# Kernel tuning notes

Measured on AMD Instinct MI355X. Metric: run time of the kernel, lower is better.

## Reference

```python
import jax, jax.numpy as jnp
import numpy as np

HEADS = 12
WH = WW = 7
N = WH * WW  # 49 tokens per window
NW = 64      # windows per image (mask groups)


def _relative_position_index():
    ch, cw = np.meshgrid(np.arange(WH), np.arange(WW), indexing='ij')
    coords = np.stack([ch, cw]).reshape(2, -1)  # [2, N]
    rel = coords[:, :, None] - coords[:, None, :]  # [2, N, N]
    rel = rel.transpose(1, 2, 0)
    rel[:, :, 0] += WH - 1
    rel[:, :, 1] += WW - 1
    rel[:, :, 0] *= 2 * WW - 1
    return rel.sum(-1).astype(np.int32)  # [N, N]


def setup_inputs() -> dict:
    key = jax.random.key(0)
    ks = jax.random.split(key, 6)
    B, C = 4096, 384
    x = jax.random.normal(ks[0], (B, N, C), dtype=jnp.float32)
    mask = jnp.where(jax.random.uniform(ks[1], (NW, N, N)) > 0.5, 0.0, -100.0).astype(jnp.float32)
    W_qkv = jax.random.normal(ks[2], (C, 3 * C), dtype=jnp.float32) * 0.02
    b_qkv = jnp.zeros((3 * C,), dtype=jnp.float32)
    W_out = jax.random.normal(ks[3], (C, C), dtype=jnp.float32) * 0.02
    b_out = jnp.zeros((C,), dtype=jnp.float32)
    rpb_table = jax.random.normal(ks[4], ((2 * WH - 1) * (2 * WW - 1), HEADS), dtype=jnp.float32) * 0.01
    rel_index = jnp.asarray(_relative_position_index())
    return {"x": x, "mask": mask, "W_qkv": W_qkv, "b_qkv": b_qkv,
            "W_out": W_out, "b_out": b_out, "rpb_table": rpb_table,
            "rel_index": rel_index}


def reference(x, mask, W_qkv, b_qkv, W_out, b_out, rpb_table, rel_index):
    B, n, C = x.shape
    hd = C // HEADS
    scale = hd ** (-0.5)
    qkv = x @ W_qkv + b_qkv                      # [B, n, 3C]
    q, k, v = jnp.split(qkv, 3, axis=2)
    def heads(t):
        return t.reshape(B, n, HEADS, hd).transpose(0, 2, 1, 3)  # b h n d
    q = heads(q) * scale
    k = heads(k)
    v = heads(v)
    attn = jnp.einsum('bhmc,bhnc->bhmn', q, k)   # [B, h, n, n]
    bias = rpb_table[rel_index.reshape(-1)].reshape(n, n, HEADS).transpose(2, 0, 1)
    attn = attn + bias[None]
    nw = mask.shape[0]
    attn = attn.reshape(B // nw, nw, HEADS, n, n) + mask[None, :, None]
    attn = attn.reshape(B, HEADS, n, n)
    attn = jax.nn.softmax(attn, axis=3)
    out = jnp.einsum('bhmn,bhnc->bhmc', attn, v)  # [B, h, n, d]
    out = out.transpose(0, 2, 1, 3).reshape(B, n, C)
    return out @ W_out + b_out
```

## Files before the change

kernel.cpp:

```cpp
#include <hip/hip_runtime.h>

#define NTOK 49
#define CDIM 384
#define HEADS 12
#define HD 32
#define NWIN 64
#define NQKV 1152
#define SCALE 0.17677669529663687f

typedef __attribute__((ext_vector_type(8))) __bf16 bf16x8;
typedef __attribute__((ext_vector_type(4))) float f32x4;

#define OFF_WQKVT   0ull
#define OFF_WOUTT   884736ull
#define OFF_ADDEND  1179648ull
#define OFF_QKVB    8555520ull
#define OFF_ATTNOUT 470977536ull
#define OFF_XB      OFF_ATTNOUT

__device__ __forceinline__ void async_copy16(__bf16* lds_dst, const __bf16* g_src) {
    __builtin_amdgcn_global_load_lds(
        (const __attribute__((address_space(1))) void*)g_src,
        (__attribute__((address_space(3))) void*)lds_dst,
        16, 0, 0);
}


__global__ void prep_weights(const float* __restrict__ Wqkv, const float* __restrict__ Wout,
                             __bf16* __restrict__ WqkvT, __bf16* __restrict__ WoutT) {
    int idx = blockIdx.x * 256 + threadIdx.x;
    if (idx < NQKV * CDIM) {
        int n = idx / CDIM, k = idx % CDIM;
        WqkvT[idx] = (__bf16)Wqkv[(size_t)k * NQKV + n];
    }
    if (idx < CDIM * CDIM) {
        int n = idx / CDIM, k = idx % CDIM;
        WoutT[idx] = (__bf16)Wout[(size_t)k * CDIM + n];
    }
}

__global__ void prep_addend(const float* __restrict__ rpb, const int* __restrict__ rel,
                            const float* __restrict__ mask, float* __restrict__ addend) {
    int idx = blockIdx.x * 256 + threadIdx.x;
    if (idx >= NWIN * HEADS * NTOK * NTOK) return;
    int mn = idx % (NTOK * NTOK);
    int h  = (idx / (NTOK * NTOK)) % HEADS;
    int w  = idx / (NTOK * NTOK * HEADS);
    addend[idx] = rpb[rel[mn] * HEADS + h] + mask[(size_t)w * NTOK * NTOK + mn];
}

__global__ __launch_bounds__(256) void prep_xb(const float* __restrict__ x,
                                               __bf16* __restrict__ xb, int total8) {
    int stride = gridDim.x * 256;
    for (int i = blockIdx.x * 256 + threadIdx.x; i < total8; i += stride) {
        float4 a = reinterpret_cast<const float4*>(x)[i * 2];
        float4 b = reinterpret_cast<const float4*>(x)[i * 2 + 1];
        union { __bf16 h[8]; uint4 u; } t;
        t.h[0] = (__bf16)a.x; t.h[1] = (__bf16)a.y; t.h[2] = (__bf16)a.z; t.h[3] = (__bf16)a.w;
        t.h[4] = (__bf16)b.x; t.h[5] = (__bf16)b.y; t.h[6] = (__bf16)b.z; t.h[7] = (__bf16)b.w;
        reinterpret_cast<uint4*>(xb)[i] = t.u;
    }
}


__global__ __launch_bounds__(256, 3) void gemm_qkv(
    const __bf16* __restrict__ xb, const __bf16* __restrict__ WqkvT,
    const float* __restrict__ bqkv, __bf16* __restrict__ qkvb)
{
    __shared__ __attribute__((aligned(16))) __bf16 smem[16384];
    __bf16* As = smem;
    __bf16* Bs = smem + 8192;

    const int cpx  = 14112 >> 3;
    const int lid  = (blockIdx.x & 7) * cpx + (blockIdx.x >> 3);
    const int mblk = lid / 9, nblk = lid % 9;
    const int n0  = nblk * 128;
    const int bm0 = mblk * 128;

    const int tid = threadIdx.x;
    const int wave = tid >> 6, lane = tid & 63;
    const int l15 = lane & 15, l4 = lane >> 4;
    const int wr = wave >> 1, wc = wave & 1;

    f32x4 acc[4][4] = {};

    for (int k0 = 0; k0 < CDIM; k0 += 64) {
#pragma unroll
        for (int j = 0; j < 4; ++j) {
            int c = wave * 4 + j;
            int mt = c >> 1, kk = c & 1;
            const __bf16* sa = xb + (size_t)(bm0 + mt * 16 + l15) * CDIM + k0 + kk * 32 + l4 * 8;
            async_copy16(&As[c * 512], sa);
            const __bf16* sb = WqkvT + (size_t)(n0 + mt * 16 + l15) * CDIM + k0 + kk * 32 + l4 * 8;
            async_copy16(&Bs[c * 512], sb);
        }
        __syncthreads();

#pragma unroll
        for (int kk = 0; kk < 2; ++kk) {
            bf16x8 af[4], bf[4];
#pragma unroll
            for (int mi = 0; mi < 4; ++mi)
                af[mi] = *reinterpret_cast<const bf16x8*>(&As[((wr * 4 + mi) * 2 + kk) * 512 + lane * 8]);
#pragma unroll
            for (int ni = 0; ni < 4; ++ni)
                bf[ni] = *reinterpret_cast<const bf16x8*>(&Bs[((wc * 4 + ni) * 2 + kk) * 512 + lane * 8]);
#pragma unroll
            for (int mi = 0; mi < 4; ++mi)
#pragma unroll
                for (int ni = 0; ni < 4; ++ni)
                    acc[mi][ni] = __builtin_amdgcn_mfma_f32_16x16x32_bf16(af[mi], bf[ni], acc[mi][ni], 0, 0, 0);
        }
        __syncthreads();
    }

    const float scl = (n0 < CDIM) ? SCALE : 1.0f;
    float bias[4];
#pragma unroll
    for (int ni = 0; ni < 4; ++ni)
        bias[ni] = bqkv[n0 + wc * 64 + ni * 16 + l15];

    __bf16* Cs = smem;
#pragma unroll
    for (int mi = 0; mi < 4; ++mi)
#pragma unroll
        for (int ni = 0; ni < 4; ++ni)
#pragma unroll
            for (int r = 0; r < 4; ++r) {
                int row = wr * 64 + mi * 16 + l4 * 4 + r;
                int col = wc * 64 + ni * 16 + l15;
                int byte = (row * 256 + col * 2) ^ (((row >> 2) & 3) << 5);
                *reinterpret_cast<__bf16*>(reinterpret_cast<char*>(Cs) + byte) =
                    (__bf16)((acc[mi][ni][r] + bias[ni]) * scl);
            }
    __syncthreads();

#pragma unroll
    for (int it = 0; it < 8; ++it) {
        int idx = it * 4096 + tid * 16;
        int row = idx >> 8, bcol = idx & 255;
        int sb = (row * 256 + bcol) ^ (((row >> 2) & 3) << 5);
        uint4 v = *reinterpret_cast<const uint4*>(reinterpret_cast<const char*>(Cs) + sb);
        *reinterpret_cast<uint4*>(reinterpret_cast<char*>(&qkvb[(size_t)(bm0 + row) * NQKV + n0]) + bcol) = v;
    }
}


__global__ __launch_bounds__(256) void attn(
    const __bf16* __restrict__ qkvb, const float* __restrict__ addend,
    __bf16* __restrict__ attnout)
{
    __shared__ __attribute__((aligned(16))) __bf16 ps[4][2][64][8];
    const int b = blockIdx.x;
    const int tid = threadIdx.x;
    const int wave = tid >> 6, lane = tid & 63;
    const int l15 = lane & 15, l4 = lane >> 4;
    const int h = blockIdx.y * 4 + wave;
    const int w = b & (NWIN - 1);

    const __bf16* base = qkvb + (size_t)b * NTOK * NQKV;

    bf16x8 kf[4];
#pragma unroll
    for (int nt = 0; nt < 4; ++nt)
        kf[nt] = *reinterpret_cast<const bf16x8*>(base + (size_t)(nt * 16 + l15) * NQKV + CDIM + h * HD + l4 * 8);

    bf16x8 vf[2][2];
#pragma unroll
    for (int dt = 0; dt < 2; ++dt)
#pragma unroll
        for (int kb = 0; kb < 2; ++kb)
#pragma unroll
            for (int j = 0; j < 8; ++j) {
                int tok = kb * 32 + l4 * 8 + j;
                vf[dt][kb][j] = base[(size_t)tok * NQKV + 2 * CDIM + h * HD + dt * 16 + l15];
            }

    const float* add_h = addend + (size_t)(w * HEADS + h) * (NTOK * NTOK);

    for (int mt = 0; mt < 4; ++mt) {
        bf16x8 qf = *reinterpret_cast<const bf16x8*>(base + (size_t)(mt * 16 + l15) * NQKV + h * HD + l4 * 8);
        f32x4 s[4];
#pragma unroll
        for (int nt = 0; nt < 4; ++nt) {
            f32x4 z = {};
            s[nt] = __builtin_amdgcn_mfma_f32_16x16x32_bf16(qf, kf[nt], z, 0, 0, 0);
        }

#pragma unroll
        for (int r = 0; r < 4; ++r) {
            int m = mt * 16 + l4 * 4 + r;
            float vals[4];
#pragma unroll
            for (int nt = 0; nt < 4; ++nt) {
                int n = nt * 16 + l15;
                float sv = s[nt][r];
                if (n < NTOK) {
                    if (m < NTOK) sv += add_h[m * NTOK + n];
                } else {
                    sv = -1e30f;
                }
                vals[nt] = sv;
            }
            float mx = fmaxf(fmaxf(vals[0], vals[1]), fmaxf(vals[2], vals[3]));
            mx = fmaxf(mx, __shfl_xor(mx, 1));
            mx = fmaxf(mx, __shfl_xor(mx, 2));
            mx = fmaxf(mx, __shfl_xor(mx, 4));
            mx = fmaxf(mx, __shfl_xor(mx, 8));
            float e0 = __expf(vals[0] - mx);
            float e1 = __expf(vals[1] - mx);
            float e2 = __expf(vals[2] - mx);
            float e3 = __expf(vals[3] - mx);
            float sum = (e0 + e1) + (e2 + e3);
            sum += __shfl_xor(sum, 1);
            sum += __shfl_xor(sum, 2);
            sum += __shfl_xor(sum, 4);
            sum += __shfl_xor(sum, 8);
            float inv = 1.0f / sum;
            float ev[4] = {e0, e1, e2, e3};
#pragma unroll
            for (int nt = 0; nt < 4; ++nt) {
                int lp = (l4 * 4 + r) + 16 * ((nt & 1) * 2 + (l15 >> 3));
                ps[wave][nt >> 1][lp][l15 & 7] = (__bf16)(ev[nt] * inv);
            }
        }

        f32x4 o[2] = {};
#pragma unroll
        for (int kb = 0; kb < 2; ++kb) {
            bf16x8 ap = *reinterpret_cast<const bf16x8*>(&ps[wave][kb][lane][0]);
#pragma unroll
            for (int dt = 0; dt < 2; ++dt)
                o[dt] = __builtin_amdgcn_mfma_f32_16x16x32_bf16(ap, vf[dt][kb], o[dt], 0, 0, 0);
        }
#pragma unroll
        for (int dt = 0; dt < 2; ++dt) {
            int col = h * HD + dt * 16 + l15;
#pragma unroll
            for (int r = 0; r < 4; ++r) {
                int tok = mt * 16 + l4 * 4 + r;
                if (tok < NTOK)
                    attnout[((size_t)b * NTOK + tok) * CDIM + col] = (__bf16)o[dt][r];
            }
        }
    }
}


__global__ __launch_bounds__(256, 3) void out_proj(
    const __bf16* __restrict__ A, const __bf16* __restrict__ WoutT,
    const float* __restrict__ bout, float* __restrict__ out)
{
    __shared__ __attribute__((aligned(16))) __bf16 as[4 * 12 * 512];
    const int blk = blockIdx.x, tid = threadIdx.x;
    const int wave = tid >> 6, lane = tid & 63;
    const int l15 = lane & 15, l4 = lane >> 4;

    const __bf16* Ab = A + (size_t)blk * 64 * CDIM;
    for (int i = tid; i < 64 * CDIM / 8; i += 256) {
        int4 ld = reinterpret_cast<const int4*>(Ab)[i];
        int e = i * 8;
        int row = e / CDIM, c = e % CDIM;
        int mt = row >> 4, kb = c >> 5;
        int lp = (row & 15) + 16 * ((c & 31) >> 3);
        int slot = lp ^ (kb & 7);
        *reinterpret_cast<int4*>(&as[((mt * 12 + kb) * 64 + slot) * 8]) = ld;
    }
    __syncthreads();

    f32x4 acc[6][4] = {};
    for (int kb = 0; kb < 12; ++kb) {
        int slot = lane ^ (kb & 7);
        bf16x8 af[4];
#pragma unroll
        for (int mt = 0; mt < 4; ++mt)
            af[mt] = *reinterpret_cast<const bf16x8*>(&as[((mt * 12 + kb) * 64 + slot) * 8]);
#pragma unroll
        for (int j = 0; j < 6; ++j) {
            int col = (wave * 6 + j) * 16 + l15;
            bf16x8 bf = *reinterpret_cast<const bf16x8*>(WoutT + (size_t)col * CDIM + kb * 32 + l4 * 8);
#pragma unroll
            for (int mt = 0; mt < 4; ++mt)
                acc[j][mt] = __builtin_amdgcn_mfma_f32_16x16x32_bf16(af[mt], bf, acc[j][mt], 0, 0, 0);
        }
    }
#pragma unroll
    for (int j = 0; j < 6; ++j) {
        int col = (wave * 6 + j) * 16 + l15;
        float bias = bout[col];
#pragma unroll
        for (int mt = 0; mt < 4; ++mt) {
#pragma unroll
            for (int r = 0; r < 4; ++r) {
                size_t row = (size_t)blk * 64 + mt * 16 + l4 * 4 + r;
                out[row * CDIM + col] = acc[j][mt][r] + bias;
            }
        }
    }
}


extern "C" void kernel_launch(void* const* d_in, const int* in_sizes, int n_in,
                              void* d_out, int out_size, void* d_ws, size_t ws_size,
                              hipStream_t stream) {
    (void)n_in; (void)out_size; (void)ws_size;
    const float* x    = (const float*)d_in[0];
    const float* mask = (const float*)d_in[1];
    const float* Wqkv = (const float*)d_in[2];
    const float* bqkv = (const float*)d_in[3];
    const float* Wout = (const float*)d_in[4];
    const float* bout = (const float*)d_in[5];
    const float* rpb  = (const float*)d_in[6];
    const int*   rel  = (const int*)d_in[7];

    const int B = in_sizes[0] / (NTOK * CDIM);
    const int M = B * NTOK;

    char* ws = (char*)d_ws;
    __bf16* WqkvT   = (__bf16*)(ws + OFF_WQKVT);
    __bf16* WoutT   = (__bf16*)(ws + OFF_WOUTT);
    float*  addend  = (float*)(ws + OFF_ADDEND);
    __bf16* qkvb    = (__bf16*)(ws + OFF_QKVB);
    __bf16* xb      = (__bf16*)(ws + OFF_XB);
    __bf16* attnout = (__bf16*)(ws + OFF_ATTNOUT);
    float*  out     = (float*)d_out;

    prep_weights<<<(NQKV * CDIM + 255) / 256, 256, 0, stream>>>(Wqkv, Wout, WqkvT, WoutT);
    prep_addend<<<(NWIN * HEADS * NTOK * NTOK + 255) / 256, 256, 0, stream>>>(rpb, rel, mask, addend);
    prep_xb<<<2048, 256, 0, stream>>>(x, xb, M * CDIM / 8);
    gemm_qkv<<<(M / 128) * (NQKV / 128), 256, 0, stream>>>(xb, WqkvT, bqkv, qkvb);
    attn<<<dim3(B, 3), 256, 0, stream>>>(qkvb, addend, attnout);
    out_proj<<<M / 64, 256, 0, stream>>>(attnout, WoutT, bout, out);
}
```

Before: 939.9 us.

## Fuse window attention with output projection, keeping attention output in LDS

Merges the attention and output-projection kernels into one kernel with one block per window. Each wave loops over three heads and writes its attention output straight into a swizzled LDS tile, which then feeds the Wout GEMM. This removes the bf16 attnout round trip through global memory and one kernel launch. In exchange, grid parallelism drops from B×3 to B blocks, and each block now handles all 12 heads serially across its waves. The projection GEMM also does padded work on 64 rows per window to produce 49 valid rows, where before it ran on dense 64-row tiles.

```diff
diff --git a/kernel.cpp b/kernel.cpp
--- a/kernel.cpp
+++ b/kernel.cpp
@@ -15,8 +15,7 @@
 #define OFF_WOUTT   884736ull
 #define OFF_ADDEND  1179648ull
 #define OFF_QKVB    8555520ull
-#define OFF_ATTNOUT 470977536ull
-#define OFF_XB      OFF_ATTNOUT
+#define OFF_XB      470977536ull
 
 __device__ __forceinline__ void async_copy16(__bf16* lds_dst, const __bf16* g_src) {
     __builtin_amdgcn_global_load_lds(
@@ -146,125 +145,107 @@
 }
 
 
-__global__ __launch_bounds__(256) void attn(
+__global__ __launch_bounds__(256) void attn_oproj(
     const __bf16* __restrict__ qkvb, const float* __restrict__ addend,
-    __bf16* __restrict__ attnout)
+    const __bf16* __restrict__ WoutT, const float* __restrict__ bout,
+    float* __restrict__ out)
 {
+    __shared__ __attribute__((aligned(16))) __bf16 ao[4 * 12 * 512];
     __shared__ __attribute__((aligned(16))) __bf16 ps[4][2][64][8];
     const int b = blockIdx.x;
     const int tid = threadIdx.x;
     const int wave = tid >> 6, lane = tid & 63;
     const int l15 = lane & 15, l4 = lane >> 4;
-    const int h = blockIdx.y * 4 + wave;
     const int w = b & (NWIN - 1);
 
     const __bf16* base = qkvb + (size_t)b * NTOK * NQKV;
 
-    bf16x8 kf[4];
-#pragma unroll
-    for (int nt = 0; nt < 4; ++nt)
-        kf[nt] = *reinterpret_cast<const bf16x8*>(base + (size_t)(nt * 16 + l15) * NQKV + CDIM + h * HD + l4 * 8);
-
-    bf16x8 vf[2][2];
-#pragma unroll
-    for (int dt = 0; dt < 2; ++dt)
-#pragma unroll
-        for (int kb = 0; kb < 2; ++kb)
-#pragma unroll
-            for (int j = 0; j < 8; ++j) {
-                int tok = kb * 32 + l4 * 8 + j;
-                vf[dt][kb][j] = base[(size_t)tok * NQKV + 2 * CDIM + h * HD + dt * 16 + l15];
-            }
-
-    const float* add_h = addend + (size_t)(w * HEADS + h) * (NTOK * NTOK);
-
-    for (int mt = 0; mt < 4; ++mt) {
-        bf16x8 qf = *reinterpret_cast<const bf16x8*>(base + (size_t)(mt * 16 + l15) * NQKV + h * HD + l4 * 8);
-        f32x4 s[4];
-#pragma unroll
-        for (int nt = 0; nt < 4; ++nt) {
-            f32x4 z = {};
-            s[nt] = __builtin_amdgcn_mfma_f32_16x16x32_bf16(qf, kf[nt], z, 0, 0, 0);
-        }
-
-#pragma unroll
-        for (int r = 0; r < 4; ++r) {
-            int m = mt * 16 + l4 * 4 + r;
-            float vals[4];
+    for (int hi = 0; hi < 3; ++hi) {
+        const int h = hi * 4 + wave;
+
+        bf16x8 kf[4];
+#pragma unroll
+        for (int nt = 0; nt < 4; ++nt)
+            kf[nt] = *reinterpret_cast<const bf16x8*>(base + (size_t)(nt * 16 + l15) * NQKV + CDIM + h * HD + l4 * 8);
+
+        bf16x8 vf[2][2];
+#pragma unroll
+        for (int dt = 0; dt < 2; ++dt)
+#pragma unroll
+            for (int kb = 0; kb < 2; ++kb)
+#pragma unroll
+                for (int j = 0; j < 8; ++j) {
+                    int tok = kb * 32 + l4 * 8 + j;
+                    vf[dt][kb][j] = base[(size_t)tok * NQKV + 2 * CDIM + h * HD + dt * 16 + l15];
+                }
+
+        const float* add_h = addend + (size_t)(w * HEADS + h) * (NTOK * NTOK);
+
+        for (int mt = 0; mt < 4; ++mt) {
+            bf16x8 qf = *reinterpret_cast<const bf16x8*>(base + (size_t)(mt * 16 + l15) * NQKV + h * HD + l4 * 8);
+            f32x4 s[4];
 #pragma unroll
             for (int nt = 0; nt < 4; ++nt) {
-                int n = nt * 16 + l15;
-                float sv = s[nt][r];
-                if (n < NTOK) {
-                    if (m < NTOK) sv += add_h[m * NTOK + n];
-                } else {
-                    sv = -1e30f;
+                f32x4 z = {};
+                s[nt] = __builtin_amdgcn_mfma_f32_16x16x32_bf16(qf, kf[nt], z, 0, 0, 0);
+            }
+
+#pragma unroll
+            for (int r = 0; r < 4; ++r) {
+                int m = mt * 16 + l4 * 4 + r;
+                float vals[4];
+#pragma unroll
+                for (int nt = 0; nt < 4; ++nt) {
+                    int n = nt * 16 + l15;
+                    float sv = s[nt][r];
+                    if (n < NTOK) {
+                        if (m < NTOK) sv += add_h[m * NTOK + n];
+                    } else {
+                        sv = -1e30f;
+                    }
+                    vals[nt] = sv;
                 }
-                vals[nt] = sv;
-            }
-            float mx = fmaxf(fmaxf(vals[0], vals[1]), fmaxf(vals[2], vals[3]));
-            mx = fmaxf(mx, __shfl_xor(mx, 1));
-            mx = fmaxf(mx, __shfl_xor(mx, 2));
-            mx = fmaxf(mx, __shfl_xor(mx, 4));
-            mx = fmaxf(mx, __shfl_xor(mx, 8));
-            float e0 = __expf(vals[0] - mx);
-            float e1 = __expf(vals[1] - mx);
-            float e2 = __expf(vals[2] - mx);
-            float e3 = __expf(vals[3] - mx);
-            float sum = (e0 + e1) + (e2 + e3);
-            sum += __shfl_xor(sum, 1);
-            sum += __shfl_xor(sum, 2);
-            sum += __shfl_xor(sum, 4);
-            sum += __shfl_xor(sum, 8);
-            float inv = 1.0f / sum;
-            float ev[4] = {e0, e1, e2, e3};
-#pragma unroll
-            for (int nt = 0; nt < 4; ++nt) {
-                int lp = (l4 * 4 + r) + 16 * ((nt & 1) * 2 + (l15 >> 3));
-                ps[wave][nt >> 1][lp][l15 & 7] = (__bf16)(ev[nt] * inv);
-            }
-        }
-
-        f32x4 o[2] = {};
-#pragma unroll
-        for (int kb = 0; kb < 2; ++kb) {
-            bf16x8 ap = *reinterpret_cast<const bf16x8*>(&ps[wave][kb][lane][0]);
-#pragma unroll
-            for (int dt = 0; dt < 2; ++dt)
-                o[dt] = __builtin_amdgcn_mfma_f32_16x16x32_bf16(ap, vf[dt][kb], o[dt], 0, 0, 0);
-        }
-#pragma unroll
-        for (int dt = 0; dt < 2; ++dt) {
-            int col = h * HD + dt * 16 + l15;
-#pragma unroll
-            for (int r = 0; r < 4; ++r) {
-                int tok = mt * 16 + l4 * 4 + r;
-                if (tok < NTOK)
-                    attnout[((size_t)b * NTOK + tok) * CDIM + col] = (__bf16)o[dt][r];
-            }
-        }
-    }
-}
-
-
-__global__ __launch_bounds__(256, 3) void out_proj(
-    const __bf16* __restrict__ A, const __bf16* __restrict__ WoutT,
-    const float* __restrict__ bout, float* __restrict__ out)
-{
-    __shared__ __attribute__((aligned(16))) __bf16 as[4 * 12 * 512];
-    const int blk = blockIdx.x, tid = threadIdx.x;
-    const int wave = tid >> 6, lane = tid & 63;
-    const int l15 = lane & 15, l4 = lane >> 4;
-
-    const __bf16* Ab = A + (size_t)blk * 64 * CDIM;
-    for (int i = tid; i < 64 * CDIM / 8; i += 256) {
-        int4 ld = reinterpret_cast<const int4*>(Ab)[i];
-        int e = i * 8;
-        int row = e / CDIM, c = e % CDIM;
-        int mt = row >> 4, kb = c >> 5;
-        int lp = (row & 15) + 16 * ((c & 31) >> 3);
-        int slot = lp ^ (kb & 7);
-        *reinterpret_cast<int4*>(&as[((mt * 12 + kb) * 64 + slot) * 8]) = ld;
+                float mx = fmaxf(fmaxf(vals[0], vals[1]), fmaxf(vals[2], vals[3]));
+                mx = fmaxf(mx, __shfl_xor(mx, 1));
+                mx = fmaxf(mx, __shfl_xor(mx, 2));
+                mx = fmaxf(mx, __shfl_xor(mx, 4));
+                mx = fmaxf(mx, __shfl_xor(mx, 8));
+                float e0 = __expf(vals[0] - mx);
+                float e1 = __expf(vals[1] - mx);
+                float e2 = __expf(vals[2] - mx);
+                float e3 = __expf(vals[3] - mx);
+                float sum = (e0 + e1) + (e2 + e3);
+                sum += __shfl_xor(sum, 1);
+                sum += __shfl_xor(sum, 2);
+                sum += __shfl_xor(sum, 4);
+                sum += __shfl_xor(sum, 8);
+                float inv = 1.0f / sum;
+                float ev[4] = {e0, e1, e2, e3};
+#pragma unroll
+                for (int nt = 0; nt < 4; ++nt) {
+                    int lp = (l4 * 4 + r) + 16 * ((nt & 1) * 2 + (l15 >> 3));
+                    ps[wave][nt >> 1][lp][l15 & 7] = (__bf16)(ev[nt] * inv);
+                }
+            }
+
+            f32x4 o[2] = {};
+#pragma unroll
+            for (int kb = 0; kb < 2; ++kb) {
+                bf16x8 ap = *reinterpret_cast<const bf16x8*>(&ps[wave][kb][lane][0]);
+#pragma unroll
+                for (int dt = 0; dt < 2; ++dt)
+                    o[dt] = __builtin_amdgcn_mfma_f32_16x16x32_bf16(ap, vf[dt][kb], o[dt], 0, 0, 0);
+            }
+#pragma unroll
+            for (int dt = 0; dt < 2; ++dt) {
+#pragma unroll
+                for (int r = 0; r < 4; ++r) {
+                    int lp = (l4 * 4 + r) + 16 * (dt * 2 + (l15 >> 3));
+                    int slot = lp ^ (h & 7);
+                    ao[((mt * 12 + h) * 64 + slot) * 8 + (l15 & 7)] = (__bf16)o[dt][r];
+                }
+            }
+        }
     }
     __syncthreads();
 
@@ -274,7 +255,7 @@
         bf16x8 af[4];
 #pragma unroll
         for (int mt = 0; mt < 4; ++mt)
-            af[mt] = *reinterpret_cast<const bf16x8*>(&as[((mt * 12 + kb) * 64 + slot) * 8]);
+            af[mt] = *reinterpret_cast<const bf16x8*>(&ao[((mt * 12 + kb) * 64 + slot) * 8]);
 #pragma unroll
         for (int j = 0; j < 6; ++j) {
             int col = (wave * 6 + j) * 16 + l15;
@@ -292,8 +273,9 @@
         for (int mt = 0; mt < 4; ++mt) {
 #pragma unroll
             for (int r = 0; r < 4; ++r) {
-                size_t row = (size_t)blk * 64 + mt * 16 + l4 * 4 + r;
-                out[row * CDIM + col] = acc[j][mt][r] + bias;
+                int tok = mt * 16 + l4 * 4 + r;
+                if (tok < NTOK)
+                    out[((size_t)b * NTOK + tok) * CDIM + col] = acc[j][mt][r] + bias;
             }
         }
     }
@@ -322,13 +304,11 @@
     float*  addend  = (float*)(ws + OFF_ADDEND);
     __bf16* qkvb    = (__bf16*)(ws + OFF_QKVB);
     __bf16* xb      = (__bf16*)(ws + OFF_XB);
-    __bf16* attnout = (__bf16*)(ws + OFF_ATTNOUT);
     float*  out     = (float*)d_out;
 
     prep_weights<<<(NQKV * CDIM + 255) / 256, 256, 0, stream>>>(Wqkv, Wout, WqkvT, WoutT);
     prep_addend<<<(NWIN * HEADS * NTOK * NTOK + 255) / 256, 256, 0, stream>>>(rpb, rel, mask, addend);
     prep_xb<<<2048, 256, 0, stream>>>(x, xb, M * CDIM / 8);
     gemm_qkv<<<(M / 128) * (NQKV / 128), 256, 0, stream>>>(xb, WqkvT, bqkv, qkvb);
-    attn<<<dim3(B, 3), 256, 0, stream>>>(qkvb, addend, attnout);
-    out_proj<<<M / 64, 256, 0, stream>>>(attnout, WoutT, bout, out);
-}
+    attn_oproj<<<B, 256, 0, stream>>>(qkvb, addend, WoutT, bout, out);
+}
```

Result: slower. 1.221 ms (+29.9%).
